# Optimization experiments

Measured on AMD Instinct MI355X. Metric: run time of the kernel, lower is better.

## Reference

```python
import jax, jax.numpy as jnp
import numpy as np

D_MODEL = 1024
D_INNER = 4096
K = 127
B, L = 2, 4096

def setup_inputs() -> dict:
    key = jax.random.key(0)
    k1, k2, k3, k4, k5 = jax.random.split(key, 5)
    x = jax.random.normal(k1, (B, L, D_MODEL), dtype=jnp.float32)
    # in_proj: Linear(d, 2*m) -> weight [2m, d] (torch convention)
    w_in = jax.random.normal(k2, (2 * D_INNER, D_MODEL), dtype=jnp.float32) * (1.0 / np.sqrt(D_MODEL))
    # depthwise conv weight: [m, 1, k] in torch; store as [m, k]
    w_dw = jax.random.normal(k3, (D_INNER, K), dtype=jnp.float32) * (1.0 / np.sqrt(K))
    b_dw = jax.random.normal(k4, (D_INNER,), dtype=jnp.float32) * 0.01
    # out_proj: Linear(m, d) -> weight [d, m]
    w_out = jax.random.normal(k5, (D_MODEL, D_INNER), dtype=jnp.float32) * (1.0 / np.sqrt(D_INNER))
    return {"x": x, "w_in": w_in, "w_dw": w_dw, "b_dw": b_dw, "w_out": w_out}

def _causal_dwconv(v, w_dw, b_dw):
    # v: [B, L, m]; causal depthwise conv with kernel K
    # pad K-1 on the left only (equivalent to torch pad=K-1 then [..., :L])
    v_bcl = jnp.transpose(v, (0, 2, 1))  # [B, m, L]
    out = jax.lax.conv_general_dilated(
        v_bcl,
        w_dw[:, None, :],  # [m, 1, K]
        window_strides=(1,),
        padding=[(K - 1, 0)],
        feature_group_count=D_INNER,
        dimension_numbers=("NCH", "OIH", "NCH"),
    )
    out = out + b_dw[None, :, None]
    return jnp.transpose(out, (0, 2, 1))  # [B, L, m]

def reference(x, w_in, w_dw, b_dw, w_out):
    vg = jnp.einsum("bld,ed->ble", x, w_in)  # [B, L, 2m]
    v, g = jnp.split(vg, 2, axis=-1)
    v = _causal_dwconv(v, w_dw, b_dw)
    y = jax.nn.silu(v) * jax.nn.silu(g)
    return jnp.einsum("blm,dm->bld", y, w_out)
```

## Files before the change

### kernel.cpp

```cpp
#include <hip/hip_runtime.h>
#include <hip/hip_bf16.h>
#include <cstdint>
#include <cstddef>

typedef __fp16 f16_t;
typedef __attribute__((ext_vector_type(8))) __fp16 f16x8;
typedef __attribute__((ext_vector_type(4))) __fp16 f16x4;
typedef __attribute__((ext_vector_type(2))) __fp16 h2_t;
typedef __attribute__((ext_vector_type(4))) float floatx4;

__device__ __forceinline__ void async_copy_16B(const void* g, void* l) {
  __builtin_amdgcn_global_load_lds(
      (const __attribute__((address_space(1))) void*)g,
      (__attribute__((address_space(3))) void*)l, 16, 0, 0);
}

__global__ __launch_bounds__(256) void prep(
    const float* __restrict__ x, const float* __restrict__ w_in,
    const float* __restrict__ w_out, const float* __restrict__ w_dw,
    f16_t* __restrict__ x_h, f16_t* __restrict__ wi_h,
    f16_t* __restrict__ wo_h, h2_t* __restrict__ wp) {
  const int tid = blockIdx.x * 256 + threadIdx.x;
  if (tid < 5242880) {
    const float* src;
    f16_t* dst;
    int off;
    if (tid < 2097152) {
      src = x; dst = x_h; off = tid;
    } else if (tid < 4194304) {
      src = w_in; dst = wi_h; off = tid - 2097152;
    } else {
      src = w_out; dst = wo_h; off = tid - 4194304;
    }
    const float4 v = *(const float4*)(src + (size_t)off * 4);
    f16x4 o;
    o.x = (f16_t)v.x; o.y = (f16_t)v.y; o.z = (f16_t)v.z; o.w = (f16_t)v.w;
    *(f16x4*)(dst + (size_t)off * 4) = o;
  } else {
    const int idx = tid - 5242880;
    if (idx < 128 * 4096) {
      const int p = idx >> 12;
      const int c = idx & 4095;
      float a, b;
      if (p < 126) {
        a = w_dw[c * 127 + p]; b = w_dw[c * 127 + p + 1];
      } else if (p == 126) {
        a = w_dw[c * 127 + 126]; b = 0.f;
      } else {
        a = 0.f; b = w_dw[c * 127 + 0];
      }
      h2_t w;
      w.x = (f16_t)a; w.y = (f16_t)b;
      wp[idx] = w;
    }
  }
}

__global__ __launch_bounds__(512, 2) void gemm256_1p(
    const f16_t* __restrict__ A, const f16_t* __restrict__ B,
    f16_t* __restrict__ C, int M, int N, int K) {
  extern __shared__ char smem[];
  const int t = threadIdx.x;
  const int lane = t & 63;
  const int wave = t >> 6;
  const int wm = wave >> 2;
  const int wn = wave & 3;

  const int bid = blockIdx.x;
  const int xcd = bid & 7;
  const int l = bid >> 3;
  const int quad = l >> 5;
  const int qm = (l >> 3) & 3;
  const int qn = l & 7;
  const int m0 = ((xcd >> 1) * 8 + (quad >> 1) * 4 + qm) * 256;
  const int n0 = ((xcd & 1) * 16 + (quad & 1) * 8 + qn) * 256;

  const int fr = lane & 15;
  const int ks = lane >> 4;

  auto stageTile = [&](int d, int k0) {
#pragma unroll
    for (int u = 0; u < 4; ++u) {
      const int q = u * 512 + t;
      const int row = q >> 3, slot = q & 7;
      const int col = (slot ^ (row & 7)) * 8;
      async_copy_16B(A + (size_t)(m0 + row) * K + k0 + col,
                     smem + d * 65536 + row * 128 + slot * 16);
    }
#pragma unroll
    for (int u = 0; u < 4; ++u) {
      const int q = u * 512 + t;
      const int row = q >> 3, slot = q & 7;
      const int col = (slot ^ (row & 7)) * 8;
      async_copy_16B(B + (size_t)(n0 + row) * K + k0 + col,
                     smem + d * 65536 + 32768 + row * 128 + slot * 16);
    }
  };
  auto ldA = [&](int d, int R, int kslot) -> f16x8 {
    return *(const f16x8*)(smem + d * 65536 + R * 128 +
                           ((kslot ^ (R & 7)) << 4));
  };
  auto ldB = [&](int d, int R, int kslot) -> f16x8 {
    return *(const f16x8*)(smem + d * 65536 + 32768 + R * 128 +
                           ((kslot ^ (R & 7)) << 4));
  };

  floatx4 acc[8][4] = {};
  const int kTiles = K / 64;

  stageTile(0, 0);
  for (int tt = 0; tt < kTiles; ++tt) {
    const int d = tt & 1;
    const bool pf = (tt + 1 < kTiles);
    if (pf) {
      stageTile(d ^ 1, (tt + 1) * 64);
      asm volatile("s_waitcnt vmcnt(8)" ::: "memory");
    } else {
      asm volatile("s_waitcnt vmcnt(0)" ::: "memory");
    }
    __builtin_amdgcn_s_barrier();

    f16x8 bf[4][2];
#pragma unroll
    for (int j = 0; j < 4; ++j)
#pragma unroll
      for (int kh = 0; kh < 2; ++kh)
        bf[j][kh] = ldB(d, wn * 64 + j * 16 + fr, kh * 4 + ks);
    __builtin_amdgcn_s_setprio(1);
#pragma unroll
    for (int ii = 0; ii < 8; ++ii) {
      const f16x8 af0 = ldA(d, wm * 128 + ii * 16 + fr, ks);
      const f16x8 af1 = ldA(d, wm * 128 + ii * 16 + fr, 4 + ks);
#pragma unroll
      for (int j = 0; j < 4; ++j)
        acc[ii][j] = __builtin_amdgcn_mfma_f32_16x16x32_f16(
            af0, bf[j][0], acc[ii][j], 0, 0, 0);
#pragma unroll
      for (int j = 0; j < 4; ++j)
        acc[ii][j] = __builtin_amdgcn_mfma_f32_16x16x32_f16(
            af1, bf[j][1], acc[ii][j], 0, 0, 0);
    }
    __builtin_amdgcn_s_setprio(0);
    __builtin_amdgcn_s_barrier();
  }

  const int cr = (lane >> 4) * 4;
  const int cc = lane & 15;
#pragma unroll
  for (int i = 0; i < 8; ++i)
#pragma unroll
    for (int j = 0; j < 4; ++j)
#pragma unroll
      for (int r = 0; r < 4; ++r) {
        const int row = m0 + wm * 128 + i * 16 + cr + r;
        const int col = n0 + wn * 64 + j * 16 + cc;
        C[(size_t)row * N + col] = (f16_t)acc[i][j][r];
      }
}

__global__ __launch_bounds__(512, 2) void gemmN128_1p(
    const f16_t* __restrict__ A, const f16_t* __restrict__ B,
    float* __restrict__ C, int M, int N, int K) {
  extern __shared__ char smem[];
  const int t = threadIdx.x;
  const int lane = t & 63;
  const int wave = t >> 6;
  const int wm = wave >> 2;
  const int wn = wave & 3;

  const int bid = blockIdx.x;
  const int xcd = bid & 7;
  const int l = bid >> 3;
  const int m0 = (xcd * 4 + (l >> 3)) * 256;
  const int n0 = (l & 7) * 128;

  const int fr = lane & 15;
  const int ks = lane >> 4;

  auto stageTile = [&](int d, int k0) {
#pragma unroll
    for (int u = 0; u < 4; ++u) {
      const int q = u * 512 + t;
      const int row = q >> 3, slot = q & 7;
      const int col = (slot ^ (row & 7)) * 8;
      async_copy_16B(A + (size_t)(m0 + row) * K + k0 + col,
                     smem + d * 49152 + row * 128 + slot * 16);
    }
#pragma unroll
    for (int u = 0; u < 2; ++u) {
      const int q = u * 512 + t;
      const int row = q >> 3, slot = q & 7;
      const int col = (slot ^ (row & 7)) * 8;
      async_copy_16B(B + (size_t)(n0 + row) * K + k0 + col,
                     smem + d * 49152 + 32768 + row * 128 + slot * 16);
    }
  };
  auto ldA = [&](int d, int R, int kslot) -> f16x8 {
    return *(const f16x8*)(smem + d * 49152 + R * 128 +
                           ((kslot ^ (R & 7)) << 4));
  };
  auto ldB = [&](int d, int R, int kslot) -> f16x8 {
    return *(const f16x8*)(smem + d * 49152 + 32768 + R * 128 +
                           ((kslot ^ (R & 7)) << 4));
  };

  floatx4 acc[8][2] = {};
  const int kTiles = K / 64;

  stageTile(0, 0);
  for (int tt = 0; tt < kTiles; ++tt) {
    const int d = tt & 1;
    const bool pf = (tt + 1 < kTiles);
    if (pf) {
      stageTile(d ^ 1, (tt + 1) * 64);
      asm volatile("s_waitcnt vmcnt(6)" ::: "memory");
    } else {
      asm volatile("s_waitcnt vmcnt(0)" ::: "memory");
    }
    __builtin_amdgcn_s_barrier();

    f16x8 bf[2][2];
#pragma unroll
    for (int j = 0; j < 2; ++j)
#pragma unroll
      for (int kh = 0; kh < 2; ++kh)
        bf[j][kh] = ldB(d, wn * 32 + j * 16 + fr, kh * 4 + ks);
    __builtin_amdgcn_s_setprio(1);
#pragma unroll
    for (int ii = 0; ii < 8; ++ii) {
      const f16x8 af0 = ldA(d, wm * 128 + ii * 16 + fr, ks);
      const f16x8 af1 = ldA(d, wm * 128 + ii * 16 + fr, 4 + ks);
#pragma unroll
      for (int j = 0; j < 2; ++j)
        acc[ii][j] = __builtin_amdgcn_mfma_f32_16x16x32_f16(
            af0, bf[j][0], acc[ii][j], 0, 0, 0);
#pragma unroll
      for (int j = 0; j < 2; ++j)
        acc[ii][j] = __builtin_amdgcn_mfma_f32_16x16x32_f16(
            af1, bf[j][1], acc[ii][j], 0, 0, 0);
    }
    __builtin_amdgcn_s_setprio(0);
    __builtin_amdgcn_s_barrier();
  }

  const int cr = (lane >> 4) * 4;
  const int cc = lane & 15;
#pragma unroll
  for (int i = 0; i < 8; ++i)
#pragma unroll
    for (int j = 0; j < 2; ++j)
#pragma unroll
      for (int r = 0; r < 4; ++r) {
        const int row = m0 + wm * 128 + i * 16 + cr + r;
        const int col = n0 + wn * 32 + j * 16 + cc;
        C[(size_t)row * N + col] = acc[i][j][r];
      }
}

#define CONV_L 128
#define CPAIRS 127

__global__ __launch_bounds__(256) void conv_gate(
    const f16_t* __restrict__ vg, const h2_t* __restrict__ wp,
    const float* __restrict__ b_dw, f16_t* __restrict__ y) {
  __shared__ uint32_t vtp[CPAIRS * 64];
  __shared__ uint32_t wpl[128 * 64];
  const int t = threadIdx.x;
  const int lane = t & 63;
  const int wave = t >> 6;
  const int c0 = blockIdx.x * 64;
  const int b = blockIdx.y >> 2;
  const int lh = blockIdx.y & 3;

#pragma unroll
  for (int it = 0; it < 8; ++it) {
    const int q = it * 256 + t;
    async_copy_16B(wp + (size_t)(q >> 4) * 4096 + c0 + (q & 15) * 4,
                   wpl + q * 4);
  }

  const int c = c0 + lane;
  const float bias = b_dw[c];
  const uint32_t* vbase = vtp + wave * 16 * 64 + lane;
  const uint32_t* wbase = wpl + lane;

  for (int j = 0; j < 8; ++j) {
    const int l0 = lh * 1024 + j * CONV_L;

    for (int q = t; q < CPAIRS * 8; q += 256) {
      const int m = q >> 3;
      const int oc = (q & 7) * 8;
      const int le = l0 - 126 + 2 * m;
      uint4 a = make_uint4(0u, 0u, 0u, 0u);
      uint4 bb = make_uint4(0u, 0u, 0u, 0u);
      if (le >= 0) {
        const size_t base = (size_t)(b * 4096 + le) * 8192 + c0 + oc;
        a = *(const uint4*)(vg + base);
        bb = *(const uint4*)(vg + base + 8192);
      }
      const uint32_t aw[4] = {a.x, a.y, a.z, a.w};
      const uint32_t bw[4] = {bb.x, bb.y, bb.z, bb.w};
      uint32_t dw[8];
#pragma unroll
      for (int i = 0; i < 4; ++i) {
        dw[2 * i] = (aw[i] & 0xFFFFu) | (bw[i] << 16);
        dw[2 * i + 1] = (aw[i] >> 16) | (bw[i] & 0xFFFF0000u);
      }
      uint32_t* dst = vtp + q * 8;
      *(uint4*)dst = make_uint4(dw[0], dw[1], dw[2], dw[3]);
      *(uint4*)(dst + 4) = make_uint4(dw[4], dw[5], dw[6], dw[7]);
    }

    const int lb = l0 + wave * 32;
    const f16_t* gp = vg + (size_t)(b * 4096 + lb) * 8192 + 4096 + c;
    f16_t gvals[32];
#pragma unroll
    for (int i = 0; i < 32; ++i) gvals[i] = gp[(size_t)i * 8192];

    __syncthreads();

    float acc[32];
#pragma unroll
    for (int i = 0; i < 32; ++i) acc[i] = bias;

    h2_t ring[17];
#pragma unroll
    for (int m = 0; m < 17; ++m)
      ring[m] = __builtin_bit_cast(h2_t, vbase[m * 64]);

    {
      const h2_t w0 = __builtin_bit_cast(h2_t, wbase[127 * 64]);
#pragma unroll
      for (int h = 0; h < 16; ++h)
        acc[2 * h + 1] =
            __builtin_amdgcn_fdot2(w0, ring[h], acc[2 * h + 1], false);
    }

#pragma unroll
    for (int k = 0; k < 64; ++k) {
      const h2_t we = __builtin_bit_cast(h2_t, wbase[(2 * k) * 64]);
#pragma unroll
      for (int h = 0; h < 16; ++h)
        acc[2 * h] =
            __builtin_amdgcn_fdot2(we, ring[(k + h) % 17], acc[2 * h], false);
      if (k < 63) {
        const h2_t wo = __builtin_bit_cast(h2_t, wbase[(2 * k + 1) * 64]);
#pragma unroll
        for (int h = 0; h < 16; ++h)
          acc[2 * h + 1] = __builtin_amdgcn_fdot2(wo, ring[(k + 1 + h) % 17],
                                                  acc[2 * h + 1], false);
        if (k < 62)
          ring[k % 17] = __builtin_bit_cast(h2_t, vbase[(17 + k) * 64]);
      }
    }

    f16_t* yp = y + (size_t)(b * 4096 + lb) * 4096 + c;
#pragma unroll
    for (int i = 0; i < 32; ++i) {
      const float gv = (float)gvals[i];
      const float v = acc[i];
      const float sv = v / (1.f + __expf(-v));
      const float sg = gv / (1.f + __expf(-gv));
      yp[(size_t)i * 4096] = (f16_t)(sv * sg);
    }

    __syncthreads();
  }
}

extern "C" void kernel_launch(void* const* d_in, const int* in_sizes, int n_in,
                              void* d_out, int out_size, void* d_ws,
                              size_t ws_size, hipStream_t stream) {
  const float* x     = (const float*)d_in[0];
  const float* w_in  = (const float*)d_in[1];
  const float* w_dw  = (const float*)d_in[2];
  const float* b_dw  = (const float*)d_in[3];
  const float* w_out = (const float*)d_in[4];
  float* out = (float*)d_out;

  char* p = (char*)d_ws;
  f16_t* x_h  = (f16_t*)p; p += (size_t)8192 * 1024 * 2;
  f16_t* wi_h = (f16_t*)p; p += (size_t)8192 * 1024 * 2;
  f16_t* wo_h = (f16_t*)p; p += (size_t)1024 * 4096 * 2;
  h2_t*  wp   = (h2_t*)p;  p += (size_t)128 * 4096 * 4;
  f16_t* vg   = (f16_t*)p; p += (size_t)8192 * 8192 * 2;
  f16_t* y    = (f16_t*)p; p += (size_t)8192 * 4096 * 2;

  prep<<<22528, 256, 0, stream>>>(x, w_in, w_out, w_dw, x_h, wi_h, wo_h, wp);

  hipFuncSetAttribute(reinterpret_cast<const void*>(gemm256_1p),
                      hipFuncAttributeMaxDynamicSharedMemorySize, 131072);
  gemm256_1p<<<1024, 512, 131072, stream>>>(x_h, wi_h, vg, 8192, 8192, 1024);

  conv_gate<<<dim3(64, 8), 256, 0, stream>>>(vg, wp, b_dw, y);

  hipFuncSetAttribute(reinterpret_cast<const void*>(gemmN128_1p),
                      hipFuncAttributeMaxDynamicSharedMemorySize, 98304);
  gemmN128_1p<<<256, 512, 98304, stream>>>(y, wo_h, out, 8192, 1024, 4096);
}
```

Baseline: 452.0 us.

## Switch GEMMs to 32x32x16 MFMA with fragment-ordered LDS layout

Both GEMM kernels now use the 32x32x16 f16 MFMA instead of 16x16x32. The LDS staging layout is rewritten so each 32-row by 8-element fragment is contiguous per lane, which removes the XOR swizzle and lets each lane read its operand with a simple lane*16 offset. The larger MFMA shape cuts the number of LDS fragment loads per FLOP, at the cost of 16-wide accumulators and a different epilogue mapping. The first GEMM is also split into two launches of 512 blocks using a block-id offset, which may add launch overhead or change tail behaviour.

```diff
diff --git a/kernel.cpp b/kernel.cpp
--- a/kernel.cpp
+++ b/kernel.cpp
@@ -8,6 +8,7 @@
 typedef __attribute__((ext_vector_type(4))) __fp16 f16x4;
 typedef __attribute__((ext_vector_type(2))) __fp16 h2_t;
 typedef __attribute__((ext_vector_type(4))) float floatx4;
+typedef __attribute__((ext_vector_type(16))) float floatx16;
 
 __device__ __forceinline__ void async_copy_16B(const void* g, void* l) {
   __builtin_amdgcn_global_load_lds(
@@ -56,9 +57,9 @@
   }
 }
 
-__global__ __launch_bounds__(512, 2) void gemm256_1p(
+__global__ __launch_bounds__(512, 2) void gemm256_x32(
     const f16_t* __restrict__ A, const f16_t* __restrict__ B,
-    f16_t* __restrict__ C, int M, int N, int K) {
+    f16_t* __restrict__ C, int M, int N, int K, int bofs) {
   extern __shared__ char smem[];
   const int t = threadIdx.x;
   const int lane = t & 63;
@@ -66,7 +67,7 @@
   const int wm = wave >> 2;
   const int wn = wave & 3;
 
-  const int bid = blockIdx.x;
+  const int bid = blockIdx.x + bofs;
   const int xcd = bid & 7;
   const int l = bid >> 3;
   const int quad = l >> 5;
@@ -75,44 +76,44 @@
   const int m0 = ((xcd >> 1) * 8 + (quad >> 1) * 4 + qm) * 256;
   const int n0 = ((xcd & 1) * 16 + (quad & 1) * 8 + qn) * 256;
 
-  const int fr = lane & 15;
-  const int ks = lane >> 4;
-
   auto stageTile = [&](int d, int k0) {
+    char* base = smem + d * 65536;
 #pragma unroll
     for (int u = 0; u < 4; ++u) {
       const int q = u * 512 + t;
-      const int row = q >> 3, slot = q & 7;
-      const int col = (slot ^ (row & 7)) * 8;
-      async_copy_16B(A + (size_t)(m0 + row) * K + k0 + col,
-                     smem + d * 65536 + row * 128 + slot * 16);
+      const int frag = q >> 6;
+      const int i = q & 63;
+      const int row = (frag >> 2) * 32 + (i & 31);
+      const int col = (frag & 3) * 16 + (i >> 5) * 8;
+      async_copy_16B(A + (size_t)(m0 + row) * K + k0 + col, base + q * 16);
     }
 #pragma unroll
     for (int u = 0; u < 4; ++u) {
       const int q = u * 512 + t;
-      const int row = q >> 3, slot = q & 7;
-      const int col = (slot ^ (row & 7)) * 8;
+      const int frag = q >> 6;
+      const int i = q & 63;
+      const int row = (frag >> 2) * 32 + (i & 31);
+      const int col = (frag & 3) * 16 + (i >> 5) * 8;
       async_copy_16B(B + (size_t)(n0 + row) * K + k0 + col,
-                     smem + d * 65536 + 32768 + row * 128 + slot * 16);
-    }
-  };
-  auto ldA = [&](int d, int R, int kslot) -> f16x8 {
-    return *(const f16x8*)(smem + d * 65536 + R * 128 +
-                           ((kslot ^ (R & 7)) << 4));
-  };
-  auto ldB = [&](int d, int R, int kslot) -> f16x8 {
-    return *(const f16x8*)(smem + d * 65536 + 32768 + R * 128 +
-                           ((kslot ^ (R & 7)) << 4));
-  };
-
-  floatx4 acc[8][4] = {};
-  const int kTiles = K / 64;
+                     base + 32768 + q * 16);
+    }
+  };
+  auto ldA = [&](int d, int rb, int ks) -> f16x8 {
+    return *(const f16x8*)(smem + d * 65536 + (rb * 4 + ks) * 1024 +
+                           lane * 16);
+  };
+  auto ldB = [&](int d, int nb, int ks) -> f16x8 {
+    return *(const f16x8*)(smem + d * 65536 + 32768 + (nb * 4 + ks) * 1024 +
+                           lane * 16);
+  };
+
+  floatx16 acc[4][2] = {};
+  const int kT = K / 64;
 
   stageTile(0, 0);
-  for (int tt = 0; tt < kTiles; ++tt) {
+  for (int tt = 0; tt < kT; ++tt) {
     const int d = tt & 1;
-    const bool pf = (tt + 1 < kTiles);
-    if (pf) {
+    if (tt + 1 < kT) {
       stageTile(d ^ 1, (tt + 1) * 64);
       asm volatile("s_waitcnt vmcnt(8)" ::: "memory");
     } else {
@@ -120,45 +121,43 @@
     }
     __builtin_amdgcn_s_barrier();
 
-    f16x8 bf[4][2];
-#pragma unroll
-    for (int j = 0; j < 4; ++j)
-#pragma unroll
-      for (int kh = 0; kh < 2; ++kh)
-        bf[j][kh] = ldB(d, wn * 64 + j * 16 + fr, kh * 4 + ks);
+    f16x8 bfr[2][4];
+#pragma unroll
+    for (int nb = 0; nb < 2; ++nb)
+#pragma unroll
+      for (int ks = 0; ks < 4; ++ks)
+        bfr[nb][ks] = ldB(d, wn * 2 + nb, ks);
     __builtin_amdgcn_s_setprio(1);
 #pragma unroll
-    for (int ii = 0; ii < 8; ++ii) {
-      const f16x8 af0 = ldA(d, wm * 128 + ii * 16 + fr, ks);
-      const f16x8 af1 = ldA(d, wm * 128 + ii * 16 + fr, 4 + ks);
-#pragma unroll
-      for (int j = 0; j < 4; ++j)
-        acc[ii][j] = __builtin_amdgcn_mfma_f32_16x16x32_f16(
-            af0, bf[j][0], acc[ii][j], 0, 0, 0);
-#pragma unroll
-      for (int j = 0; j < 4; ++j)
-        acc[ii][j] = __builtin_amdgcn_mfma_f32_16x16x32_f16(
-            af1, bf[j][1], acc[ii][j], 0, 0, 0);
-    }
+    for (int ks = 0; ks < 4; ++ks)
+#pragma unroll
+      for (int i = 0; i < 4; ++i) {
+        const f16x8 af = ldA(d, wm * 4 + i, ks);
+#pragma unroll
+        for (int j = 0; j < 2; ++j)
+          acc[i][j] = __builtin_amdgcn_mfma_f32_32x32x16_f16(
+              af, bfr[j][ks], acc[i][j], 0, 0, 0);
+      }
     __builtin_amdgcn_s_setprio(0);
     __builtin_amdgcn_s_barrier();
   }
 
-  const int cr = (lane >> 4) * 4;
-  const int cc = lane & 15;
-#pragma unroll
-  for (int i = 0; i < 8; ++i)
-#pragma unroll
-    for (int j = 0; j < 4; ++j)
-#pragma unroll
-      for (int r = 0; r < 4; ++r) {
-        const int row = m0 + wm * 128 + i * 16 + cr + r;
-        const int col = n0 + wn * 64 + j * 16 + cc;
+  const int rl4 = (lane >> 5) * 4;
+  const int cl = lane & 31;
+#pragma unroll
+  for (int i = 0; i < 4; ++i)
+#pragma unroll
+    for (int j = 0; j < 2; ++j)
+#pragma unroll
+      for (int r = 0; r < 16; ++r) {
+        const int row =
+            m0 + wm * 128 + i * 32 + (r & 3) + 8 * (r >> 2) + rl4;
+        const int col = n0 + wn * 64 + j * 32 + cl;
         C[(size_t)row * N + col] = (f16_t)acc[i][j][r];
       }
 }
 
-__global__ __launch_bounds__(512, 2) void gemmN128_1p(
+__global__ __launch_bounds__(512, 2) void gemmN128_x32(
     const f16_t* __restrict__ A, const f16_t* __restrict__ B,
     float* __restrict__ C, int M, int N, int K) {
   extern __shared__ char smem[];
@@ -174,44 +173,44 @@
   const int m0 = (xcd * 4 + (l >> 3)) * 256;
   const int n0 = (l & 7) * 128;
 
-  const int fr = lane & 15;
-  const int ks = lane >> 4;
-
   auto stageTile = [&](int d, int k0) {
+    char* base = smem + d * 49152;
 #pragma unroll
     for (int u = 0; u < 4; ++u) {
       const int q = u * 512 + t;
-      const int row = q >> 3, slot = q & 7;
-      const int col = (slot ^ (row & 7)) * 8;
-      async_copy_16B(A + (size_t)(m0 + row) * K + k0 + col,
-                     smem + d * 49152 + row * 128 + slot * 16);
+      const int frag = q >> 6;
+      const int i = q & 63;
+      const int row = (frag >> 2) * 32 + (i & 31);
+      const int col = (frag & 3) * 16 + (i >> 5) * 8;
+      async_copy_16B(A + (size_t)(m0 + row) * K + k0 + col, base + q * 16);
     }
 #pragma unroll
     for (int u = 0; u < 2; ++u) {
       const int q = u * 512 + t;
-      const int row = q >> 3, slot = q & 7;
-      const int col = (slot ^ (row & 7)) * 8;
+      const int frag = q >> 6;
+      const int i = q & 63;
+      const int row = (frag >> 2) * 32 + (i & 31);
+      const int col = (frag & 3) * 16 + (i >> 5) * 8;
       async_copy_16B(B + (size_t)(n0 + row) * K + k0 + col,
-                     smem + d * 49152 + 32768 + row * 128 + slot * 16);
-    }
-  };
-  auto ldA = [&](int d, int R, int kslot) -> f16x8 {
-    return *(const f16x8*)(smem + d * 49152 + R * 128 +
-                           ((kslot ^ (R & 7)) << 4));
-  };
-  auto ldB = [&](int d, int R, int kslot) -> f16x8 {
-    return *(const f16x8*)(smem + d * 49152 + 32768 + R * 128 +
-                           ((kslot ^ (R & 7)) << 4));
-  };
-
-  floatx4 acc[8][2] = {};
-  const int kTiles = K / 64;
+                     base + 32768 + q * 16);
+    }
+  };
+  auto ldA = [&](int d, int rb, int ks) -> f16x8 {
+    return *(const f16x8*)(smem + d * 49152 + (rb * 4 + ks) * 1024 +
+                           lane * 16);
+  };
+  auto ldB = [&](int d, int nb, int ks) -> f16x8 {
+    return *(const f16x8*)(smem + d * 49152 + 32768 + (nb * 4 + ks) * 1024 +
+                           lane * 16);
+  };
+
+  floatx16 acc[4] = {};
+  const int kT = K / 64;
 
   stageTile(0, 0);
-  for (int tt = 0; tt < kTiles; ++tt) {
+  for (int tt = 0; tt < kT; ++tt) {
     const int d = tt & 1;
-    const bool pf = (tt + 1 < kTiles);
-    if (pf) {
+    if (tt + 1 < kT) {
       stageTile(d ^ 1, (tt + 1) * 64);
       asm volatile("s_waitcnt vmcnt(6)" ::: "memory");
     } else {
@@ -219,42 +218,32 @@
     }
     __builtin_amdgcn_s_barrier();
 
-    f16x8 bf[2][2];
-#pragma unroll
-    for (int j = 0; j < 2; ++j)
-#pragma unroll
-      for (int kh = 0; kh < 2; ++kh)
-        bf[j][kh] = ldB(d, wn * 32 + j * 16 + fr, kh * 4 + ks);
+    f16x8 bfr[4];
+#pragma unroll
+    for (int ks = 0; ks < 4; ++ks) bfr[ks] = ldB(d, wn, ks);
     __builtin_amdgcn_s_setprio(1);
 #pragma unroll
-    for (int ii = 0; ii < 8; ++ii) {
-      const f16x8 af0 = ldA(d, wm * 128 + ii * 16 + fr, ks);
-      const f16x8 af1 = ldA(d, wm * 128 + ii * 16 + fr, 4 + ks);
-#pragma unroll
-      for (int j = 0; j < 2; ++j)
-        acc[ii][j] = __builtin_amdgcn_mfma_f32_16x16x32_f16(
-            af0, bf[j][0], acc[ii][j], 0, 0, 0);
-#pragma unroll
-      for (int j = 0; j < 2; ++j)
-        acc[ii][j] = __builtin_amdgcn_mfma_f32_16x16x32_f16(
-            af1, bf[j][1], acc[ii][j], 0, 0, 0);
-    }
+    for (int ks = 0; ks < 4; ++ks)
+#pragma unroll
+      for (int i = 0; i < 4; ++i) {
+        const f16x8 af = ldA(d, wm * 4 + i, ks);
+        acc[i] = __builtin_amdgcn_mfma_f32_32x32x16_f16(
+            af, bfr[ks], acc[i], 0, 0, 0);
+      }
     __builtin_amdgcn_s_setprio(0);
     __builtin_amdgcn_s_barrier();
   }
 
-  const int cr = (lane >> 4) * 4;
-  const int cc = lane & 15;
-#pragma unroll
-  for (int i = 0; i < 8; ++i)
-#pragma unroll
-    for (int j = 0; j < 2; ++j)
-#pragma unroll
-      for (int r = 0; r < 4; ++r) {
-        const int row = m0 + wm * 128 + i * 16 + cr + r;
-        const int col = n0 + wn * 32 + j * 16 + cc;
-        C[(size_t)row * N + col] = acc[i][j][r];
-      }
+  const int rl4 = (lane >> 5) * 4;
+  const int cl = lane & 31;
+#pragma unroll
+  for (int i = 0; i < 4; ++i)
+#pragma unroll
+    for (int r = 0; r < 16; ++r) {
+      const int row = m0 + wm * 128 + i * 32 + (r & 3) + 8 * (r >> 2) + rl4;
+      const int col = n0 + wn * 32 + cl;
+      C[(size_t)row * N + col] = acc[i][r];
+    }
 }
 
 #define CONV_L 128
@@ -388,13 +377,16 @@
 
   prep<<<22528, 256, 0, stream>>>(x, w_in, w_out, w_dw, x_h, wi_h, wo_h, wp);
 
-  hipFuncSetAttribute(reinterpret_cast<const void*>(gemm256_1p),
+  hipFuncSetAttribute(reinterpret_cast<const void*>(gemm256_x32),
                       hipFuncAttributeMaxDynamicSharedMemorySize, 131072);
-  gemm256_1p<<<1024, 512, 131072, stream>>>(x_h, wi_h, vg, 8192, 8192, 1024);
+  gemm256_x32<<<512, 512, 131072, stream>>>(x_h, wi_h, vg, 8192, 8192, 1024,
+                                            0);
+  gemm256_x32<<<512, 512, 131072, stream>>>(x_h, wi_h, vg, 8192, 8192, 1024,
+                                            512);
 
   conv_gate<<<dim3(64, 8), 256, 0, stream>>>(vg, wp, b_dw, y);
 
-  hipFuncSetAttribute(reinterpret_cast<const void*>(gemmN128_1p),
+  hipFuncSetAttribute(reinterpret_cast<const void*>(gemmN128_x32),
                       hipFuncAttributeMaxDynamicSharedMemorySize, 98304);
-  gemmN128_1p<<<256, 512, 98304, stream>>>(y, wo_h, out, 8192, 1024, 4096);
-}
+  gemmN128_x32<<<256, 512, 98304, stream>>>(y, wo_h, out, 8192, 1024, 4096);
+}
```

After: 496.3 us. 9.8% more time.
